# Optimization experiments

Measured on AMD Instinct MI355X. Metric: run time of the kernel, lower is better.

The kernel has to match this reference:

```python
import jax, jax.numpy as jnp
import numpy as np

MARGIN = 0.2
EPS = 1e-6


def setup_inputs() -> dict:
    key = jax.random.key(0)
    k1, k2 = jax.random.split(key)
    B, C = 8192, 1024
    z_label = jax.random.randint(k1, (B,), 0, 256, dtype=jnp.int64 if jax.config.jax_enable_x64 else jnp.int32)
    z_idx = jnp.arange(B, dtype=z_label.dtype)
    z = jax.random.normal(k2, (B, C), dtype=jnp.float32)
    return {"z_label": z_label, "z_idx": z_idx, "z": z}


def reference(z_label, z_idx, z):
    B = z.shape[0]
    k = max(2, int(B * 0.01))  # static: labels overwritten if batch has a single unique label
    all_same = jnp.all(z_label == z_label[0])
    z_label = jnp.where(all_same & (jnp.arange(B) < k), -1, z_label)

    # Vectorized triplet mining (replaces per-sample Python loop):
    # positive: first j with same label, different sample idx; negative: first j with different label.
    label_eq = z_label[:, None] == z_label[None, :]            # [B, B]
    pos_mask = label_eq & (z_idx[:, None] != z_idx[None, :])   # [B, B]
    neg_mask = ~label_eq                                       # [B, B]
    pos_idx = jnp.argmax(pos_mask, axis=1)  # first True (torch.where(...)[0][0])
    neg_idx = jnp.argmax(neg_mask, axis=1)
    valid = pos_mask.any(axis=1) & neg_mask.any(axis=1)        # [B]

    # TripletMarginLoss (p=2, swap=False): d(x,y) = ||x - y + eps||_2
    a, p_emb, n_emb = z, z[pos_idx], z[neg_idx]
    d_ap = jnp.sqrt(jnp.sum((a - p_emb + EPS) ** 2, axis=1))
    d_an = jnp.sqrt(jnp.sum((a - n_emb + EPS) ** 2, axis=1))
    per = jnp.maximum(d_ap - d_an + MARGIN, 0.0)               # [B]

    n_valid = valid.sum()
    vf = valid.astype(per.dtype)
    loss = jnp.where(n_valid > 0,
                     jnp.sum(per * vf) / jnp.maximum(n_valid, 1).astype(per.dtype),
                     jnp.array(0.0, per.dtype))
    return loss
```

## Files before the change

### kernel.cpp

```cpp
#include <hip/hip_runtime.h>

#define MARGIN 0.2f
#define EPSC 1e-6f
#define INF_I 0x7fffffff
#define NB 1024

__global__ __launch_bounds__(1024) void mine_kernel(
    const int* __restrict__ label, const int* __restrict__ zidx, int B,
    int* __restrict__ g_pos, int* __restrict__ g_neg, int* __restrict__ g_valid)
{
    __shared__ int s_label[8192];
    __shared__ int s_first[258];
    __shared__ int s_second[258];
    __shared__ int s_fd_orig;
    __shared__ int s_fd_eff;
    const int tid = threadIdx.x;
    const int T   = blockDim.x;

    if (tid < 258) { s_first[tid] = INF_I; s_second[tid] = INF_I; }
    if (tid == 0) { s_fd_orig = INF_I; s_fd_eff = INF_I; }
    for (int j = tid; j < B; j += T) s_label[j] = label[j];
    __syncthreads();

    const int l0 = s_label[0];
    int lm = INF_I;
    for (int j = tid; j < B; j += T) { if (s_label[j] != l0) { lm = j; break; } }
    if (lm != INF_I) atomicMin(&s_fd_orig, lm);
    __syncthreads();

    const bool all_same = (s_fd_orig == INF_I);
    int k = B / 100; if (k < 2) k = 2;
    if (all_same) { for (int j = tid; j < k && j < B; j += T) s_label[j] = -1; }
    __syncthreads();

    const int l0e = s_label[0];
    lm = INF_I;
    for (int j = tid; j < B; j += T) {
        int l = s_label[j];
        atomicMin(&s_first[l + 1], j);
        if (l != l0e && j < lm) lm = j;
    }
    if (lm != INF_I) atomicMin(&s_fd_eff, lm);
    __syncthreads();

    for (int j = tid; j < B; j += T) {
        int l = s_label[j];
        if (j != s_first[l + 1]) atomicMin(&s_second[l + 1], j);
    }
    __syncthreads();

    const int fd = s_fd_eff;
    for (int i = tid; i < B; i += T) {
        int l  = s_label[i];
        int fo = s_first[l + 1];
        int myidx = zidx[i];
        int pos; bool vp;
        if (zidx[fo] != myidx) { pos = fo; vp = true; }
        else {
            int so = s_second[l + 1];
            if (so != INF_I) { pos = so; vp = true; }
            else             { pos = 0;  vp = false; }
        }
        int neg; bool vn;
        if (l != l0e)        { neg = 0;  vn = true; }
        else if (fd != INF_I){ neg = fd; vn = true; }
        else                 { neg = 0;  vn = false; }
        g_pos[i] = pos; g_neg[i] = neg; g_valid[i] = (vp && vn) ? 1 : 0;
    }
}

__global__ __launch_bounds__(256) void dist_kernel(
    const float* __restrict__ z, const int* __restrict__ g_pos,
    const int* __restrict__ g_neg, const int* __restrict__ g_valid,
    int B, int C, float* __restrict__ g_bsum, float* __restrict__ g_bcnt)
{
    const int wave = threadIdx.x >> 6;
    const int lane = threadIdx.x & 63;
    const int wpb  = blockDim.x >> 6;
    const int gwave  = blockIdx.x * wpb + wave;
    const int nwaves = gridDim.x * wpb;

    float lsum = 0.f, lcnt = 0.f;
    for (int i = gwave; i < B; i += nwaves) {
        const float* a = z + (size_t)i * C;
        const float* p = z + (size_t)g_pos[i] * C;
        const float* n = z + (size_t)g_neg[i] * C;
        float sap = 0.f, san = 0.f;
        const int nk = C >> 8;
        for (int k = 0; k < nk; ++k) {
            int c = ((k << 6) + lane) << 2;
            float4 av = *(const float4*)(a + c);
            float4 pv = *(const float4*)(p + c);
            float4 nv = *(const float4*)(n + c);
            float d;
            d = av.x - pv.x + EPSC; sap += d * d;
            d = av.y - pv.y + EPSC; sap += d * d;
            d = av.z - pv.z + EPSC; sap += d * d;
            d = av.w - pv.w + EPSC; sap += d * d;
            d = av.x - nv.x + EPSC; san += d * d;
            d = av.y - nv.y + EPSC; san += d * d;
            d = av.z - nv.z + EPSC; san += d * d;
            d = av.w - nv.w + EPSC; san += d * d;
        }
        for (int off = 32; off; off >>= 1) {
            sap += __shfl_xor(sap, off, 64);
            san += __shfl_xor(san, off, 64);
        }
        if (lane == 0 && g_valid[i]) {
            lsum += fmaxf(sqrtf(sap) - sqrtf(san) + MARGIN, 0.f);
            lcnt += 1.f;
        }
    }

    __shared__ float s_sum[4], s_cnt[4];
    if (lane == 0) { s_sum[wave] = lsum; s_cnt[wave] = lcnt; }
    __syncthreads();
    if (threadIdx.x == 0) {
        float bs = 0.f, bc = 0.f;
        for (int w = 0; w < wpb; ++w) { bs += s_sum[w]; bc += s_cnt[w]; }
        g_bsum[blockIdx.x] = bs;
        g_bcnt[blockIdx.x] = bc;
    }
}

__global__ __launch_bounds__(256) void final_kernel(
    const float* __restrict__ g_bsum, const float* __restrict__ g_bcnt,
    int nb, float* __restrict__ out)
{
    const int t = threadIdx.x;
    float s = 0.f, c = 0.f;
    for (int i = t; i < nb; i += blockDim.x) { s += g_bsum[i]; c += g_bcnt[i]; }
    for (int off = 32; off; off >>= 1) {
        s += __shfl_xor(s, off, 64);
        c += __shfl_xor(c, off, 64);
    }
    __shared__ float s_s[4], s_c[4];
    const int wave = t >> 6, lane = t & 63;
    if (lane == 0) { s_s[wave] = s; s_c[wave] = c; }
    __syncthreads();
    if (t == 0) {
        float ts = 0.f, tc = 0.f;
        for (int w = 0; w < 4; ++w) { ts += s_s[w]; tc += s_c[w]; }
        out[0] = (tc > 0.f) ? ts / tc : 0.f;
    }
}

extern "C" void kernel_launch(void* const* d_in, const int* in_sizes, int n_in,
                              void* d_out, int out_size, void* d_ws, size_t ws_size,
                              hipStream_t stream) {
    const int*   z_label = (const int*)d_in[0];
    const int*   z_idx   = (const int*)d_in[1];
    const float* z       = (const float*)d_in[2];
    const int B = in_sizes[0];
    const int C = in_sizes[2] / B;
    float* out = (float*)d_out;

    char* base = (char*)d_ws;
    float* g_bsum = (float*)base;
    float* g_bcnt = g_bsum + NB;
    int*   g_pos   = (int*)(g_bcnt + NB);
    int*   g_neg   = g_pos + B;
    int*   g_valid = g_neg + B;

    mine_kernel<<<1, 1024, 0, stream>>>(z_label, z_idx, B, g_pos, g_neg, g_valid);
    dist_kernel<<<NB, 256, 0, stream>>>(z, g_pos, g_neg, g_valid, B, C,
                                        g_bsum, g_bcnt);
    final_kernel<<<1, 256, 0, stream>>>(g_bsum, g_bcnt, NB, out);
}
```

Before: 98.92 us.

## Assign one row per wave in dist kernel, unroll loads, vectorize label load

The distance kernel now launches one wave per row (B/4 blocks) instead of a grid-stride loop over 1024 blocks. For C==1024 it issues all twelve float4 loads up front, so more memory requests are in flight per wave. The single-block mining kernel loads labels with int4 vector reads. The trade-off is a larger grid and a longer partial-sum array for the final reduction to walk.

```diff
diff --git a/kernel.cpp b/kernel.cpp
--- a/kernel.cpp
+++ b/kernel.cpp
@@ -3,7 +3,6 @@
 #define MARGIN 0.2f
 #define EPSC 1e-6f
 #define INF_I 0x7fffffff
-#define NB 1024
 
 __global__ __launch_bounds__(1024) void mine_kernel(
     const int* __restrict__ label, const int* __restrict__ zidx, int B,
@@ -19,7 +18,14 @@
 
     if (tid < 258) { s_first[tid] = INF_I; s_second[tid] = INF_I; }
     if (tid == 0) { s_fd_orig = INF_I; s_fd_eff = INF_I; }
-    for (int j = tid; j < B; j += T) s_label[j] = label[j];
+    if ((B & 3) == 0) {
+        for (int j = tid * 4; j < B; j += T * 4) {
+            int4 v = *(const int4*)(label + j);
+            s_label[j] = v.x; s_label[j+1] = v.y; s_label[j+2] = v.z; s_label[j+3] = v.w;
+        }
+    } else {
+        for (int j = tid; j < B; j += T) s_label[j] = label[j];
+    }
     __syncthreads();
 
     const int l0 = s_label[0];
@@ -69,6 +75,19 @@
     }
 }
 
+__device__ inline void acc8(const float4& av, const float4& pv, const float4& nv,
+                            float& sap, float& san) {
+    float d;
+    d = av.x - pv.x + EPSC; sap += d * d;
+    d = av.y - pv.y + EPSC; sap += d * d;
+    d = av.z - pv.z + EPSC; sap += d * d;
+    d = av.w - pv.w + EPSC; sap += d * d;
+    d = av.x - nv.x + EPSC; san += d * d;
+    d = av.y - nv.y + EPSC; san += d * d;
+    d = av.z - nv.z + EPSC; san += d * d;
+    d = av.w - nv.w + EPSC; san += d * d;
+}
+
 __global__ __launch_bounds__(256) void dist_kernel(
     const float* __restrict__ z, const int* __restrict__ g_pos,
     const int* __restrict__ g_neg, const int* __restrict__ g_valid,
@@ -76,39 +95,41 @@
 {
     const int wave = threadIdx.x >> 6;
     const int lane = threadIdx.x & 63;
-    const int wpb  = blockDim.x >> 6;
-    const int gwave  = blockIdx.x * wpb + wave;
-    const int nwaves = gridDim.x * wpb;
+    const int i = blockIdx.x * 4 + wave;
 
     float lsum = 0.f, lcnt = 0.f;
-    for (int i = gwave; i < B; i += nwaves) {
-        const float* a = z + (size_t)i * C;
-        const float* p = z + (size_t)g_pos[i] * C;
-        const float* n = z + (size_t)g_neg[i] * C;
+    if (i < B) {
+        const float4* a = (const float4*)(z + (size_t)i * C) + lane;
+        const float4* p = (const float4*)(z + (size_t)g_pos[i] * C) + lane;
+        const float4* n = (const float4*)(z + (size_t)g_neg[i] * C) + lane;
         float sap = 0.f, san = 0.f;
-        const int nk = C >> 8;
-        for (int k = 0; k < nk; ++k) {
-            int c = ((k << 6) + lane) << 2;
-            float4 av = *(const float4*)(a + c);
-            float4 pv = *(const float4*)(p + c);
-            float4 nv = *(const float4*)(n + c);
-            float d;
-            d = av.x - pv.x + EPSC; sap += d * d;
-            d = av.y - pv.y + EPSC; sap += d * d;
-            d = av.z - pv.z + EPSC; sap += d * d;
-            d = av.w - pv.w + EPSC; sap += d * d;
-            d = av.x - nv.x + EPSC; san += d * d;
-            d = av.y - nv.y + EPSC; san += d * d;
-            d = av.z - nv.z + EPSC; san += d * d;
-            d = av.w - nv.w + EPSC; san += d * d;
+        if (C == 1024) {
+            float4 a0 = a[0], a1 = a[64], a2 = a[128], a3 = a[192];
+            float4 p0 = p[0], p1 = p[64], p2 = p[128], p3 = p[192];
+            float4 n0 = n[0], n1 = n[64], n2 = n[128], n3 = n[192];
+            acc8(a0, p0, n0, sap, san);
+            acc8(a1, p1, n1, sap, san);
+            acc8(a2, p2, n2, sap, san);
+            acc8(a3, p3, n3, sap, san);
+        } else {
+            const int nk = C >> 8;
+            for (int k = 0; k < nk; ++k)
+                acc8(a[k * 64], p[k * 64], n[k * 64], sap, san);
+            for (int c = (nk << 8) + lane; c < C; c += 64) {
+                float av = z[(size_t)i * C + c];
+                float pv = z[(size_t)g_pos[i] * C + c];
+                float nv = z[(size_t)g_neg[i] * C + c];
+                float d = av - pv + EPSC; sap += d * d;
+                d = av - nv + EPSC; san += d * d;
+            }
         }
         for (int off = 32; off; off >>= 1) {
             sap += __shfl_xor(sap, off, 64);
             san += __shfl_xor(san, off, 64);
         }
         if (lane == 0 && g_valid[i]) {
-            lsum += fmaxf(sqrtf(sap) - sqrtf(san) + MARGIN, 0.f);
-            lcnt += 1.f;
+            lsum = fmaxf(sqrtf(sap) - sqrtf(san) + MARGIN, 0.f);
+            lcnt = 1.f;
         }
     }
 
@@ -117,7 +138,7 @@
     __syncthreads();
     if (threadIdx.x == 0) {
         float bs = 0.f, bc = 0.f;
-        for (int w = 0; w < wpb; ++w) { bs += s_sum[w]; bc += s_cnt[w]; }
+        for (int w = 0; w < 4; ++w) { bs += s_sum[w]; bc += s_cnt[w]; }
         g_bsum[blockIdx.x] = bs;
         g_bcnt[blockIdx.x] = bc;
     }
@@ -155,15 +176,17 @@
     const int C = in_sizes[2] / B;
     float* out = (float*)d_out;
 
+    const int nblk = (B + 3) / 4;
+
     char* base = (char*)d_ws;
     float* g_bsum = (float*)base;
-    float* g_bcnt = g_bsum + NB;
-    int*   g_pos   = (int*)(g_bcnt + NB);
+    float* g_bcnt = g_bsum + nblk;
+    int*   g_pos   = (int*)(g_bcnt + nblk);
     int*   g_neg   = g_pos + B;
     int*   g_valid = g_neg + B;
 
     mine_kernel<<<1, 1024, 0, stream>>>(z_label, z_idx, B, g_pos, g_neg, g_valid);
-    dist_kernel<<<NB, 256, 0, stream>>>(z, g_pos, g_neg, g_valid, B, C,
-                                        g_bsum, g_bcnt);
-    final_kernel<<<1, 256, 0, stream>>>(g_bsum, g_bcnt, NB, out);
+    dist_kernel<<<nblk, 256, 0, stream>>>(z, g_pos, g_neg, g_valid, B, C,
+                                          g_bsum, g_bcnt);
+    final_kernel<<<1, 256, 0, stream>>>(g_bsum, g_bcnt, nblk, out);
 }
```

New measurement: 97.11 us. No clear change (-1.8%).
